# Kernel tuning notes

Hardware: AMD Instinct MI355X
Metric: run time of the kernel (lower is better)

Reference implementation:

```python
import jax, jax.numpy as jnp
import numpy as np

# --- static configuration (mirrors init_kwargs) ---
L = 16        # latent_size
HL = 512      # hypernet_layer_size
D = 64        # decoder_layer_size
NDEC = 2      # decoder_n_layers
B, G = 128, 100  # batch, grid (pressure levels)
LOGP_MEAN, LOGP_STD = 0.0, 3.0
T_MEAN, T_STD = 1500.0, 500.0

# decoder layer structure generated by the hypernet
WEIGHT_SIZES = [(1, D)] + [(D, D)] * NDEC + [(D, 1)]
BIAS_SIZES = [1] + [D] * NDEC + [1]
OUT_SIZE = sum(a * b for a, b in WEIGHT_SIZES) + sum(BIAS_SIZES)  # 8450


def setup_inputs() -> dict:
    key = jax.random.key(0)
    ks = jax.random.split(key, 8)
    def init(k, shape, fan_in):
        return (jax.random.normal(k, shape, jnp.float32) / np.float32(np.sqrt(fan_in)))
    return {
        "z": jax.random.normal(ks[0], (B, L), jnp.float32),
        "log_P": jax.random.normal(ks[1], (B, G), jnp.float32) * 2.0,
        # hypernet MLP params: L -> HL -> HL -> HL -> OUT_SIZE
        "hW0": init(ks[2], (L, HL), L), "hb0": jnp.zeros((HL,), jnp.float32),
        "hW1": init(ks[3], (HL, HL), HL), "hb1": jnp.zeros((HL,), jnp.float32),
        "hW2": init(ks[4], (HL, HL), HL), "hb2": jnp.zeros((HL,), jnp.float32),
        "hWo": init(ks[5], (HL, OUT_SIZE), HL), "hbo": jnp.zeros((OUT_SIZE,), jnp.float32),
    }


def reference(z, log_P, hW0, hb0, hW1, hb1, hW2, hb2, hWo, hbo):
    Bsz, Gsz = log_P.shape
    R = Bsz * Gsz  # flattened rows
    # broadcast latent over the pressure grid: (B, L) -> (R, L)
    z_flat = jnp.broadcast_to(z[:, None, :], (Bsz, Gsz, z.shape[-1])).reshape(R, -1)
    # normalize pressure -> decoder input, shape (R, 1)
    x = (log_P.reshape(R, 1) - LOGP_MEAN) / LOGP_STD
    # hypernet MLP (leaky_relu, slope 0.01 like torch default)
    h = jax.nn.leaky_relu(z_flat @ hW0 + hb0)
    h = jax.nn.leaky_relu(h @ hW1 + hb1)
    h = jax.nn.leaky_relu(h @ hW2 + hb2)
    wab = h @ hWo + hbo  # (R, OUT_SIZE): per-row decoder weights+biases
    # per-row decoder: chain of batched GEMVs with siren activation
    off = 0
    n_layers = len(WEIGHT_SIZES)
    for i, ((di, do), bs) in enumerate(zip(WEIGHT_SIZES, BIAS_SIZES)):
        n = di * do
        w = wab[:, off:off + n].reshape(R, di, do)
        b = wab[:, off + n:off + n + bs]  # broadcasts against (R, do)
        off += n + bs
        x = jnp.einsum('bi,bij->bj', x, w) + b
        if i == 0:
            x = x * 30.0  # siren first-layer omega_0
        if i < n_layers - 1:
            x = jnp.sin(x)  # siren activation; last layer is Identity
    T_pred = x.reshape(Bsz, Gsz)
    # undo temperature normalization
    return T_pred * T_STD + T_MEAN
```

## Files before the change

### kernel.cpp

```cpp
#include <hip/hip_runtime.h>

#define WSTRIDE 8704
#define DSTR 68

__device__ __forceinline__ float lrelu(float x) { return x > 0.0f ? x : 0.01f * x; }

__global__ __launch_bounds__(256) void h0T_kernel(const float* __restrict__ z,
                                                  const float* __restrict__ W,
                                                  const float* __restrict__ bias,
                                                  float* __restrict__ h0T) {
    int b = blockIdx.x >> 1;
    int j = (blockIdx.x & 1) * 256 + threadIdx.x;
    const float* __restrict__ zr = z + b * 16;
    float acc = bias[j];
#pragma unroll
    for (int l = 0; l < 16; ++l) acc = fmaf(zr[l], W[l * 512 + j], acc);
    h0T[j * 128 + b] = lrelu(acc);
}

__global__ __launch_bounds__(256) void gemmT_kernel(const float* __restrict__ At,
                                                    const float* __restrict__ W,
                                                    const float* __restrict__ bias,
                                                    float* __restrict__ OT) {
    __shared__ __align__(16) float red[4][64][20];
    int jt = blockIdx.x & 7;
    int bt = blockIdx.x >> 3;
    int lane = threadIdx.x & 63;
    int wid = __builtin_amdgcn_readfirstlane(threadIdx.x >> 6);
    int j = jt * 64 + lane;
    int b0 = bt * 16;
    float acc[16];
#pragma unroll
    for (int i = 0; i < 16; ++i) acc[i] = 0.f;
    int k0 = wid * 128;
#pragma unroll 4
    for (int kk = 0; kk < 128; ++kk) {
        int k = k0 + kk;
        const float* __restrict__ a = At + k * 128 + b0;
        float w = W[k * 512 + j];
#pragma unroll
        for (int i = 0; i < 16; ++i) acc[i] = fmaf(a[i], w, acc[i]);
    }
#pragma unroll
    for (int t4 = 0; t4 < 4; ++t4)
        *(float4*)&red[wid][lane][t4 * 4] = make_float4(acc[t4*4], acc[t4*4+1], acc[t4*4+2], acc[t4*4+3]);
    __syncthreads();
    int jj = threadIdx.x & 63;
    int bq = threadIdx.x >> 6;
    float4 s0 = *(const float4*)&red[0][jj][bq * 4];
    float4 s1 = *(const float4*)&red[1][jj][bq * 4];
    float4 s2 = *(const float4*)&red[2][jj][bq * 4];
    float4 s3 = *(const float4*)&red[3][jj][bq * 4];
    int jg = jt * 64 + jj;
    float bj = bias[jg];
    float4 o;
    o.x = lrelu(s0.x + s1.x + s2.x + s3.x + bj);
    o.y = lrelu(s0.y + s1.y + s2.y + s3.y + bj);
    o.z = lrelu(s0.z + s1.z + s2.z + s3.z + bj);
    o.w = lrelu(s0.w + s1.w + s2.w + s3.w + bj);
    *(float4*)&OT[jg * 128 + b0 + bq * 4] = o;
}

__global__ __launch_bounds__(256) void wabT_kernel(const float* __restrict__ At,
                                                   const float* __restrict__ W,
                                                   const float* __restrict__ bias,
                                                   float* __restrict__ wab) {
    __shared__ __align__(16) float red[4][64][20];
    int r = blockIdx.x & 7;
    int m = blockIdx.x >> 3;
    int bt = m & 7;
    int jt = (m >> 3) * 8 + r;
    if (jt >= 133) return;
    int lane = threadIdx.x & 63;
    int wid = __builtin_amdgcn_readfirstlane(threadIdx.x >> 6);
    int j = jt * 64 + lane;
    int jc = j < 8450 ? j : 8448;
    int b0 = bt * 16;
    float acc[16];
#pragma unroll
    for (int i = 0; i < 16; ++i) acc[i] = 0.f;
    int k0 = wid * 128;
#pragma unroll 4
    for (int kk = 0; kk < 128; ++kk) {
        int k = k0 + kk;
        const float* __restrict__ a = At + k * 128 + b0;
        float w = W[k * 8450 + jc];
#pragma unroll
        for (int i = 0; i < 16; ++i) acc[i] = fmaf(a[i], w, acc[i]);
    }
#pragma unroll
    for (int t4 = 0; t4 < 4; ++t4)
        *(float4*)&red[wid][lane][t4 * 4] = make_float4(acc[t4*4], acc[t4*4+1], acc[t4*4+2], acc[t4*4+3]);
    __syncthreads();
    int jj = threadIdx.x & 63;
    int bq = threadIdx.x >> 6;
    float4 s0 = *(const float4*)&red[0][jj][bq * 4];
    float4 s1 = *(const float4*)&red[1][jj][bq * 4];
    float4 s2 = *(const float4*)&red[2][jj][bq * 4];
    float4 s3 = *(const float4*)&red[3][jj][bq * 4];
    int jg = jt * 64 + jj;
    if (jg < 8450) {
        float bj = bias[jg];
        float v0 = s0.x + s1.x + s2.x + s3.x + bj;
        float v1 = s0.y + s1.y + s2.y + s3.y + bj;
        float v2 = s0.z + s1.z + s2.z + s3.z + bj;
        float v3 = s0.w + s1.w + s2.w + s3.w + bj;
        wab[(b0 + bq * 4 + 0) * WSTRIDE + jg] = v0;
        wab[(b0 + bq * 4 + 1) * WSTRIDE + jg] = v1;
        wab[(b0 + bq * 4 + 2) * WSTRIDE + jg] = v2;
        wab[(b0 + bq * 4 + 3) * WSTRIDE + jg] = v3;
    }
}

__global__ __launch_bounds__(256) void decoder_kernel(const float* __restrict__ wab,
                                                      const float* __restrict__ logP,
                                                      float* __restrict__ out) {
    __shared__ __align__(16) float hA[64 * DSTR];
    __shared__ __align__(16) float hB[64 * DSTR];
    __shared__ float red[4][68];
    int b   = blockIdx.x >> 1;
    int gbl = blockIdx.x & 1;
    int lane = threadIdx.x & 63;
    int wid  = __builtin_amdgcn_readfirstlane(threadIdx.x >> 6);
    int jq = wid * 16;
    int g = gbl * 64 + lane;
    bool act = g < 100;
    const float* __restrict__ row = wab + b * WSTRIDE;
    float x0 = act ? logP[b * 100 + g] * (1.0f / 3.0f) : 0.0f;

    float c0 = row[64];
#pragma unroll
    for (int t4 = 0; t4 < 4; ++t4) {
        float4 v;
        v.x = __sinf(30.0f * fmaf(x0, row[jq + t4*4 + 0], c0));
        v.y = __sinf(30.0f * fmaf(x0, row[jq + t4*4 + 1], c0));
        v.z = __sinf(30.0f * fmaf(x0, row[jq + t4*4 + 2], c0));
        v.w = __sinf(30.0f * fmaf(x0, row[jq + t4*4 + 3], c0));
        *(float4*)&hA[lane * DSTR + jq + t4 * 4] = v;
    }
    __syncthreads();

    {
        float a[16];
#pragma unroll
        for (int t = 0; t < 16; ++t) a[t] = row[4161 + jq + t];
        for (int i4 = 0; i4 < 16; ++i4) {
            float4 hv = *(const float4*)&hA[lane * DSTR + i4 * 4];
#pragma unroll
            for (int e = 0; e < 4; ++e) {
                int i = i4 * 4 + e;
                const float* __restrict__ wr = row + 65 + i * 64 + jq;
                float hi = (&hv.x)[e];
#pragma unroll
                for (int t = 0; t < 16; ++t) a[t] = fmaf(hi, wr[t], a[t]);
            }
        }
#pragma unroll
        for (int t4 = 0; t4 < 4; ++t4) {
            float4 v;
            v.x = __sinf(a[t4*4 + 0]); v.y = __sinf(a[t4*4 + 1]);
            v.z = __sinf(a[t4*4 + 2]); v.w = __sinf(a[t4*4 + 3]);
            *(float4*)&hB[lane * DSTR + jq + t4 * 4] = v;
        }
    }
    __syncthreads();

    {
        float a[16];
#pragma unroll
        for (int t = 0; t < 16; ++t) a[t] = row[8321 + jq + t];
        for (int i4 = 0; i4 < 16; ++i4) {
            float4 hv = *(const float4*)&hB[lane * DSTR + i4 * 4];
#pragma unroll
            for (int e = 0; e < 4; ++e) {
                int i = i4 * 4 + e;
                const float* __restrict__ wr = row + 4225 + i * 64 + jq;
                float hi = (&hv.x)[e];
#pragma unroll
                for (int t = 0; t < 16; ++t) a[t] = fmaf(hi, wr[t], a[t]);
            }
        }
#pragma unroll
        for (int t4 = 0; t4 < 4; ++t4) {
            float4 v;
            v.x = __sinf(a[t4*4 + 0]); v.y = __sinf(a[t4*4 + 1]);
            v.z = __sinf(a[t4*4 + 2]); v.w = __sinf(a[t4*4 + 3]);
            *(float4*)&hA[lane * DSTR + jq + t4 * 4] = v;
        }
    }
    __syncthreads();

    float p = 0.f;
#pragma unroll
    for (int t4 = 0; t4 < 4; ++t4) {
        float4 hv = *(const float4*)&hA[lane * DSTR + jq + t4 * 4];
        p = fmaf(hv.x, row[8385 + jq + t4*4 + 0], p);
        p = fmaf(hv.y, row[8385 + jq + t4*4 + 1], p);
        p = fmaf(hv.z, row[8385 + jq + t4*4 + 2], p);
        p = fmaf(hv.w, row[8385 + jq + t4*4 + 3], p);
    }
    red[wid][lane] = p;
    __syncthreads();
    if (wid == 0 && act) {
        float s = red[0][lane] + red[1][lane] + red[2][lane] + red[3][lane] + row[8449];
        out[b * 100 + g] = fmaf(s, 500.0f, 1500.0f);
    }
}

extern "C" void kernel_launch(void* const* d_in, const int* in_sizes, int n_in,
                              void* d_out, int out_size, void* d_ws, size_t ws_size,
                              hipStream_t stream) {
    const float* z    = (const float*)d_in[0];
    const float* logP = (const float*)d_in[1];
    const float* hW0  = (const float*)d_in[2];
    const float* hb0  = (const float*)d_in[3];
    const float* hW1  = (const float*)d_in[4];
    const float* hb1  = (const float*)d_in[5];
    const float* hW2  = (const float*)d_in[6];
    const float* hb2  = (const float*)d_in[7];
    const float* hWo  = (const float*)d_in[8];
    const float* hbo  = (const float*)d_in[9];
    float* out = (float*)d_out;

    float* wab = (float*)d_ws;
    float* h0T = wab + 128 * WSTRIDE;
    float* h1T = h0T + 512 * 128;
    float* h2T = h1T + 512 * 128;

    h0T_kernel<<<256, 256, 0, stream>>>(z, hW0, hb0, h0T);
    gemmT_kernel<<<64, 256, 0, stream>>>(h0T, hW1, hb1, h1T);
    gemmT_kernel<<<64, 256, 0, stream>>>(h1T, hW2, hb2, h2T);
    wabT_kernel<<<1088, 256, 0, stream>>>(h2T, hWo, hbo, wab);
    decoder_kernel<<<256, 256, 0, stream>>>(wab, logP, out);
}
```

Baseline: 75.47 us.

## Retile hypernet GEMM kernels and add tail block for output layer

```diff
diff --git a/kernel.cpp b/kernel.cpp
--- a/kernel.cpp
+++ b/kernel.cpp
@@ -5,110 +5,109 @@
 
 __device__ __forceinline__ float lrelu(float x) { return x > 0.0f ? x : 0.01f * x; }
 
-__global__ __launch_bounds__(256) void h0T_kernel(const float* __restrict__ z,
+__global__ __launch_bounds__(128) void h0T_kernel(const float* __restrict__ z,
                                                   const float* __restrict__ W,
                                                   const float* __restrict__ bias,
                                                   float* __restrict__ h0T) {
-    int b = blockIdx.x >> 1;
-    int j = (blockIdx.x & 1) * 256 + threadIdx.x;
-    const float* __restrict__ zr = z + b * 16;
+    int j = blockIdx.x;
+    int b = threadIdx.x;
+    float zr[16];
+    *(float4*)&zr[0]  = *(const float4*)&z[b * 16 + 0];
+    *(float4*)&zr[4]  = *(const float4*)&z[b * 16 + 4];
+    *(float4*)&zr[8]  = *(const float4*)&z[b * 16 + 8];
+    *(float4*)&zr[12] = *(const float4*)&z[b * 16 + 12];
     float acc = bias[j];
 #pragma unroll
     for (int l = 0; l < 16; ++l) acc = fmaf(zr[l], W[l * 512 + j], acc);
     h0T[j * 128 + b] = lrelu(acc);
 }
 
-__global__ __launch_bounds__(256) void gemmT_kernel(const float* __restrict__ At,
+__global__ __launch_bounds__(512) void gemmT_kernel(const float* __restrict__ At,
                                                     const float* __restrict__ W,
                                                     const float* __restrict__ bias,
                                                     float* __restrict__ OT) {
-    __shared__ __align__(16) float red[4][64][20];
+    __shared__ float red[8][64][13];
     int jt = blockIdx.x & 7;
     int bt = blockIdx.x >> 3;
     int lane = threadIdx.x & 63;
-    int wid = __builtin_amdgcn_readfirstlane(threadIdx.x >> 6);
+    int wid  = __builtin_amdgcn_readfirstlane(threadIdx.x >> 6);
     int j = jt * 64 + lane;
-    int b0 = bt * 16;
-    float acc[16];
-#pragma unroll
-    for (int i = 0; i < 16; ++i) acc[i] = 0.f;
-    int k0 = wid * 128;
-#pragma unroll 4
-    for (int kk = 0; kk < 128; ++kk) {
+    int b0 = bt * 8;
+    float acc[8] = {};
+    int k0 = wid * 64;
+#pragma unroll 4
+    for (int kk = 0; kk < 64; ++kk) {
         int k = k0 + kk;
         const float* __restrict__ a = At + k * 128 + b0;
         float w = W[k * 512 + j];
 #pragma unroll
-        for (int i = 0; i < 16; ++i) acc[i] = fmaf(a[i], w, acc[i]);
-    }
-#pragma unroll
-    for (int t4 = 0; t4 < 4; ++t4)
-        *(float4*)&red[wid][lane][t4 * 4] = make_float4(acc[t4*4], acc[t4*4+1], acc[t4*4+2], acc[t4*4+3]);
-    __syncthreads();
-    int jj = threadIdx.x & 63;
-    int bq = threadIdx.x >> 6;
-    float4 s0 = *(const float4*)&red[0][jj][bq * 4];
-    float4 s1 = *(const float4*)&red[1][jj][bq * 4];
-    float4 s2 = *(const float4*)&red[2][jj][bq * 4];
-    float4 s3 = *(const float4*)&red[3][jj][bq * 4];
+        for (int i = 0; i < 8; ++i) acc[i] = fmaf(a[i], w, acc[i]);
+    }
+#pragma unroll
+    for (int i = 0; i < 8; ++i) red[wid][lane][i] = acc[i];
+    __syncthreads();
+    int jj = threadIdx.x >> 3;
+    int bb = threadIdx.x & 7;
+    float s = 0.f;
+#pragma unroll
+    for (int w = 0; w < 8; ++w) s += red[w][jj][bb];
     int jg = jt * 64 + jj;
-    float bj = bias[jg];
-    float4 o;
-    o.x = lrelu(s0.x + s1.x + s2.x + s3.x + bj);
-    o.y = lrelu(s0.y + s1.y + s2.y + s3.y + bj);
-    o.z = lrelu(s0.z + s1.z + s2.z + s3.z + bj);
-    o.w = lrelu(s0.w + s1.w + s2.w + s3.w + bj);
-    *(float4*)&OT[jg * 128 + b0 + bq * 4] = o;
+    OT[jg * 128 + b0 + bb] = lrelu(s + bias[jg]);
 }
 
 __global__ __launch_bounds__(256) void wabT_kernel(const float* __restrict__ At,
                                                    const float* __restrict__ W,
                                                    const float* __restrict__ bias,
                                                    float* __restrict__ wab) {
-    __shared__ __align__(16) float red[4][64][20];
-    int r = blockIdx.x & 7;
-    int m = blockIdx.x >> 3;
-    int bt = m & 7;
-    int jt = (m >> 3) * 8 + r;
-    if (jt >= 133) return;
-    int lane = threadIdx.x & 63;
-    int wid = __builtin_amdgcn_readfirstlane(threadIdx.x >> 6);
-    int j = jt * 64 + lane;
-    int jc = j < 8450 ? j : 8448;
-    int b0 = bt * 16;
-    float acc[16];
-#pragma unroll
-    for (int i = 0; i < 16; ++i) acc[i] = 0.f;
+    __shared__ float red[4][128][13];
+    int tid = threadIdx.x;
+    if (blockIdx.x == 1152) {
+        int b = tid & 127;
+        int jc = 8448 + (tid >> 7);
+        float acc = 0.f;
+#pragma unroll 8
+        for (int k = 0; k < 512; ++k)
+            acc = fmaf(At[k * 128 + b], W[k * 8450 + jc], acc);
+        wab[b * WSTRIDE + jc] = acc + bias[jc];
+        return;
+    }
+    int xcd = blockIdx.x & 7;
+    int idx = blockIdx.x >> 3;
+    int jt = (idx >> 4) * 8 + xcd;
+    int bt = idx & 15;
+    if (jt >= 66) return;
+    int lane = tid & 63;
+    int wid  = __builtin_amdgcn_readfirstlane(tid >> 6);
+    int j = jt * 128 + lane * 2;
+    int b0 = bt * 8;
+    float acc[8][2] = {};
     int k0 = wid * 128;
 #pragma unroll 4
     for (int kk = 0; kk < 128; ++kk) {
         int k = k0 + kk;
         const float* __restrict__ a = At + k * 128 + b0;
-        float w = W[k * 8450 + jc];
-#pragma unroll
-        for (int i = 0; i < 16; ++i) acc[i] = fmaf(a[i], w, acc[i]);
-    }
-#pragma unroll
-    for (int t4 = 0; t4 < 4; ++t4)
-        *(float4*)&red[wid][lane][t4 * 4] = make_float4(acc[t4*4], acc[t4*4+1], acc[t4*4+2], acc[t4*4+3]);
-    __syncthreads();
-    int jj = threadIdx.x & 63;
-    int bq = threadIdx.x >> 6;
-    float4 s0 = *(const float4*)&red[0][jj][bq * 4];
-    float4 s1 = *(const float4*)&red[1][jj][bq * 4];
-    float4 s2 = *(const float4*)&red[2][jj][bq * 4];
-    float4 s3 = *(const float4*)&red[3][jj][bq * 4];
-    int jg = jt * 64 + jj;
-    if (jg < 8450) {
-        float bj = bias[jg];
-        float v0 = s0.x + s1.x + s2.x + s3.x + bj;
-        float v1 = s0.y + s1.y + s2.y + s3.y + bj;
-        float v2 = s0.z + s1.z + s2.z + s3.z + bj;
-        float v3 = s0.w + s1.w + s2.w + s3.w + bj;
-        wab[(b0 + bq * 4 + 0) * WSTRIDE + jg] = v0;
-        wab[(b0 + bq * 4 + 1) * WSTRIDE + jg] = v1;
-        wab[(b0 + bq * 4 + 2) * WSTRIDE + jg] = v2;
-        wab[(b0 + bq * 4 + 3) * WSTRIDE + jg] = v3;
+        float2 w = *(const float2*)&W[k * 8450 + j];
+#pragma unroll
+        for (int i = 0; i < 8; ++i) {
+            acc[i][0] = fmaf(a[i], w.x, acc[i][0]);
+            acc[i][1] = fmaf(a[i], w.y, acc[i][1]);
+        }
+    }
+#pragma unroll
+    for (int i = 0; i < 8; ++i) {
+        red[wid][lane * 2 + 0][i] = acc[i][0];
+        red[wid][lane * 2 + 1][i] = acc[i][1];
+    }
+    __syncthreads();
+    int jj = tid & 127;
+    int half = tid >> 7;
+    int jg = jt * 128 + jj;
+    float bj = bias[jg];
+#pragma unroll
+    for (int q = 0; q < 4; ++q) {
+        int bb = half * 4 + q;
+        float s = red[0][jj][bb] + red[1][jj][bb] + red[2][jj][bb] + red[3][jj][bb];
+        wab[(b0 + bb) * WSTRIDE + jg] = s + bj;
     }
 }
 
@@ -144,6 +143,7 @@
         float a[16];
 #pragma unroll
         for (int t = 0; t < 16; ++t) a[t] = row[4161 + jq + t];
+#pragma unroll 4
         for (int i4 = 0; i4 < 16; ++i4) {
             float4 hv = *(const float4*)&hA[lane * DSTR + i4 * 4];
 #pragma unroll
@@ -169,6 +169,7 @@
         float a[16];
 #pragma unroll
         for (int t = 0; t < 16; ++t) a[t] = row[8321 + jq + t];
+#pragma unroll 4
         for (int i4 = 0; i4 < 16; ++i4) {
             float4 hv = *(const float4*)&hB[lane * DSTR + i4 * 4];
 #pragma unroll
@@ -227,9 +228,9 @@
     float* h1T = h0T + 512 * 128;
     float* h2T = h1T + 512 * 128;
 
-    h0T_kernel<<<256, 256, 0, stream>>>(z, hW0, hb0, h0T);
-    gemmT_kernel<<<64, 256, 0, stream>>>(h0T, hW1, hb1, h1T);
-    gemmT_kernel<<<64, 256, 0, stream>>>(h1T, hW2, hb2, h2T);
-    wabT_kernel<<<1088, 256, 0, stream>>>(h2T, hWo, hbo, wab);
+    h0T_kernel<<<512, 128, 0, stream>>>(z, hW0, hb0, h0T);
+    gemmT_kernel<<<128, 512, 0, stream>>>(h0T, hW1, hb1, h1T);
+    gemmT_kernel<<<128, 512, 0, stream>>>(h1T, hW2, hb2, h2T);
+    wabT_kernel<<<1153, 256, 0, stream>>>(h2T, hWo, hbo, wab);
     decoder_kernel<<<256, 256, 0, stream>>>(wab, logP, out);
 }
```

Result: no change. 74.99 us (-0.6%).
